# Performance work log

Hardware: AMD Instinct MI355X
Metric: run time of the kernel (lower is better)

Reference implementation:

```python
import jax, jax.numpy as jnp
import numpy as np

K_NEIGHBORS = 32
BN_EPS = 1e-5


def setup_inputs() -> dict:
    key = jax.random.key(0)
    ks = jax.random.split(key, 5)
    B, N, C, OUT = 16, 2048, 3, 32
    x = jax.random.normal(ks[0], (B, N, C), dtype=jnp.float32)
    W1 = jax.random.normal(ks[1], (2 * C, 2 * C), dtype=jnp.float32) * 0.3
    b1 = jax.random.normal(ks[2], (2 * C,), dtype=jnp.float32) * 0.05
    W2 = jax.random.normal(ks[3], (2 * C, OUT), dtype=jnp.float32) * 0.3
    b2 = jax.random.normal(ks[4], (OUT,), dtype=jnp.float32) * 0.05
    return {
        "x": x,
        "W1": W1, "b1": b1,
        "gamma1": jnp.ones((2 * C,), jnp.float32), "beta1": jnp.zeros((2 * C,), jnp.float32),
        "W2": W2, "b2": b2,
        "gamma2": jnp.ones((OUT,), jnp.float32), "beta2": jnp.zeros((OUT,), jnp.float32),
    }


def _batchnorm_train(h, gamma, beta):
    # normalize over all axes except the last (channel) axis, biased variance
    axes = tuple(range(h.ndim - 1))
    mean = jnp.mean(h, axis=axes)
    var = jnp.var(h, axis=axes)
    return gamma * (h - mean) * jax.lax.rsqrt(var + BN_EPS) + beta


def reference(x, W1, b1, gamma1, beta1, W2, b2, gamma2, beta2):
    B, N, C = x.shape
    K = min(K_NEIGHBORS, N)
    # brute-force KNN: squared euclidean distances [B,N,N]
    sq = jnp.sum(x * x, axis=-1)
    d = sq[:, :, None] + sq[:, None, :] - 2.0 * jnp.einsum('bnc,bmc->bnm', x, x)
    _, idx = jax.lax.top_k(-d, K)  # [B,N,K] nearest (self first)
    # gather neighbor points: [B,N,K,C]
    knn = jax.vmap(lambda pts, i: pts[i])(x, idx)
    diffs = x[:, :, None, :] - knn
    h = jnp.concatenate([jnp.broadcast_to(x[:, :, None, :], (B, N, K, C)), diffs], axis=-1)  # [B,N,K,2C]
    h = jax.nn.elu(_batchnorm_train(h @ W1 + b1, gamma1, beta1))
    h = jnp.max(h, axis=2)  # max-pool over K neighbors -> [B,N,2C]
    y = jax.nn.elu(_batchnorm_train(h @ W2 + b2, gamma2, beta2))
    return y
```

## Files before the change

### kernel.cpp

```cpp
#include <hip/hip_runtime.h>
#include <math.h>

namespace {
constexpr int NB = 16, NP = 2048, KNN = 32, CH1 = 6, CH2 = 32;
constexpr int QPB = 8;
constexpr int NBLK = NB * NP / QPB;
constexpr float BN_EPS = 1e-5f;

constexpr size_t OFF_S1REP   = 0;
constexpr size_t OFF_STATS2L = 768;
constexpr size_t OFF_SC1     = 1664;
constexpr size_t OFF_P       = 2048;
constexpr size_t OFF_MINQ    = OFF_P + sizeof(float)*NB*NP*CH1;
}

typedef __attribute__((ext_vector_type(2))) float f32x2;

__device__ __forceinline__ f32x2 pk_mul(f32x2 a, f32x2 b) {
  f32x2 d; asm("v_pk_mul_f32 %0, %1, %2" : "=v"(d) : "v"(a), "v"(b)); return d;
}
__device__ __forceinline__ f32x2 pk_add(f32x2 a, f32x2 b) {
  f32x2 d; asm("v_pk_add_f32 %0, %1, %2" : "=v"(d) : "v"(a), "v"(b)); return d;
}

template <int C> __device__ __forceinline__ int dpp0i(int x) {
  return __builtin_amdgcn_update_dpp(0, x, C, 0xf, 0xf, true);
}
template <int C> __device__ __forceinline__ float dpp0f(float x) {
  return __uint_as_float((unsigned)__builtin_amdgcn_update_dpp(
      0, (int)__float_as_uint(x), C, 0xf, 0xf, true));
}
template <int C> __device__ __forceinline__ float dppInff(float x) {
  return __uint_as_float((unsigned)__builtin_amdgcn_update_dpp(
      0x7F800000, (int)__float_as_uint(x), C, 0xf, 0xf, false));
}
__device__ __forceinline__ int wave_isum_bcast(int x) {
  x += dpp0i<0x111>(x); x += dpp0i<0x112>(x); x += dpp0i<0x114>(x);
  x += dpp0i<0x118>(x); x += dpp0i<0x142>(x); x += dpp0i<0x143>(x);
  return __builtin_amdgcn_readlane(x, 63);
}
__device__ __forceinline__ float wave_fsum63(float x) {
  x += dpp0f<0x111>(x); x += dpp0f<0x112>(x); x += dpp0f<0x114>(x);
  x += dpp0f<0x118>(x); x += dpp0f<0x142>(x); x += dpp0f<0x143>(x);
  return x;
}
__device__ __forceinline__ float wave_fmin63(float x) {
  x = fminf(x, dppInff<0x111>(x)); x = fminf(x, dppInff<0x112>(x));
  x = fminf(x, dppInff<0x114>(x)); x = fminf(x, dppInff<0x118>(x));
  x = fminf(x, dppInff<0x142>(x)); x = fminf(x, dppInff<0x143>(x));
  return x;
}

#define BSEL(m, x, y) ((((x)) & (m)) | (((y)) & ~(m)))

#define RROUND(alive, below, rem, ca, plane)                  \
  { unsigned z_ = BSEL((plane), 0u, (alive));                 \
    int c_ = wave_isum_bcast(__popc(z_));                     \
    if (c_ >= (rem)) { alive = z_; ca = c_; }                 \
    else { rem -= c_; below |= z_; alive &= (plane); ca -= c_; } }

#define RPAIR(alive, below, rem, ca, p0, p1)                                   \
  { unsigned a0_  = BSEL((p0), 0u, (alive));                                   \
    unsigned a1_  = (alive) & (p0);                                            \
    unsigned z00_ = BSEL((p1), 0u, a0_);                                       \
    unsigned z01_ = a0_ & (p1);                                                \
    unsigned z10_ = BSEL((p1), 0u, a1_);                                       \
    unsigned z11_ = a1_ & (p1);                                                \
    int c00_ = wave_isum_bcast(__popc(z00_));                                  \
    int c01_ = wave_isum_bcast(__popc(z01_));                                  \
    int c10_ = wave_isum_bcast(__popc(z10_));                                  \
    if (c00_ >= (rem)) { alive = z00_; ca = c00_; }                            \
    else if (c00_ + c01_ >= (rem)) {                                           \
      below |= z00_; rem -= c00_; alive = z01_; ca = c01_;                     \
    } else if (c00_ + c01_ + c10_ >= (rem)) {                                  \
      below |= z00_ | z01_; rem -= c00_ + c01_; alive = z10_; ca = c10_;       \
    } else {                                                                   \
      below |= z00_ | z01_ | z10_; rem -= c00_ + c01_ + c10_;                  \
      alive = z11_; ca = (ca) - c00_ - c01_ - c10_;                            \
    } }

#define TR16(a)                                                      \
  _Pragma("unroll") for (int g_ = 0; g_ < 8; ++g_) {                 \
    unsigned hi_ = a[g_], lo_ = a[g_+8];                             \
    a[g_]   = __builtin_amdgcn_perm(hi_, lo_, 0x07030501u);          \
    a[g_+8] = __builtin_amdgcn_perm(hi_, lo_, 0x06020400u); }        \
  _Pragma("unroll") for (int g_ = 0; g_ < 8; ++g_) {                 \
    int k_ = (g_ >> 2)*8 + (g_ & 3);                                 \
    unsigned A_ = a[k_], B_ = a[k_+4];                               \
    a[k_]   = BSEL(0x0F0F0F0Fu, B_ >> 4, A_);                        \
    a[k_+4] = BSEL(0xF0F0F0F0u, A_ << 4, B_); }                      \
  _Pragma("unroll") for (int g_ = 0; g_ < 8; ++g_) {                 \
    int k_ = (g_ >> 1)*4 + (g_ & 1);                                 \
    unsigned A_ = a[k_], B_ = a[k_+2];                               \
    a[k_]   = BSEL(0x33333333u, B_ >> 2, A_);                        \
    a[k_+2] = BSEL(0xCCCCCCCCu, A_ << 2, B_); }                      \
  _Pragma("unroll") for (int g_ = 0; g_ < 8; ++g_) {                 \
    int k_ = g_*2;                                                   \
    unsigned A_ = a[k_], B_ = a[k_+1];                               \
    a[k_]   = BSEL(0x55555555u, B_ >> 1, A_);                        \
    a[k_+1] = BSEL(0xAAAAAAAAu, A_ << 1, B_); }

__global__ __launch_bounds__(512, 8) void knn_kernel(const float* __restrict__ x,
                                                     const float* __restrict__ W1,
                                                     const float* __restrict__ b1,
                                                     float* __restrict__ pout,
                                                     float* __restrict__ minq,
                                                     double* __restrict__ s1rep) {
  __shared__ float4 XC[512], YC[512], ZC[512], WC[512];
  __shared__ float red[12][QPB];
  const int lane = threadIdx.x & 63;
  const int w    = threadIdx.x >> 6;
  const int qi   = blockIdx.x * QPB + w;
  const int b    = qi >> 11;
  const int n    = qi & (NP - 1);

  const float* xb = x + (size_t)b * NP * 3;
  {
    const int t = threadIdx.x;
    const int g0 = t >> 6, ls = t & 63;
    float xx[4], yy[4], zz[4], ww[4];
#pragma unroll
    for (int k = 0; k < 4; ++k) {
      const float* pp = xb + (g0*256 + k*64 + ls) * 3;
      float a0 = pp[0], a1 = pp[1], a2 = pp[2];
      xx[k] = a0; yy[k] = a1; zz[k] = a2;
      ww[k] = __fadd_rn(__fadd_rn(__fmul_rn(a0,a0), __fmul_rn(a1,a1)), __fmul_rn(a2,a2));
    }
    XC[t] = (float4){xx[0], xx[1], xx[2], xx[3]};
    YC[t] = (float4){yy[0], yy[1], yy[2], yy[3]};
    ZC[t] = (float4){zz[0], zz[1], zz[2], zz[3]};
    WC[t] = (float4){ww[0], ww[1], ww[2], ww[3]};
  }
  __syncthreads();

  const float* Xs = (const float*)XC;
  const float* Ys = (const float*)YC;
  const float* Zs = (const float*)ZC;
  const float* Ws = (const float*)WC;

  const int vq = n >> 6, lq = n & 63;
  const int qidx = (((vq >> 2) << 6) | lq) * 4 + (vq & 3);
  const float qx = Xs[qidx], qy = Ys[qidx], qz = Zs[qidx], qw = Ws[qidx];
  const f32x2 qx2 = {qx,qx}, qy2 = {qy,qy}, qz2 = {qz,qz}, qw2 = {qw,qw};

  unsigned dd[32];
#pragma unroll
  for (int g = 0; g < 8; ++g) {
    const int cs = g*64 + lane;
    float4 X = XC[cs], Y = YC[cs], Z = ZC[cs], Wv = WC[cs];
    f32x2 x01 = {X.x,X.y}, y01 = {Y.x,Y.y}, z01 = {Z.x,Z.y}, w01 = {Wv.x,Wv.y};
    f32x2 x23 = {X.z,X.w}, y23 = {Y.z,Y.w}, z23 = {Z.z,Z.w}, w23 = {Wv.z,Wv.w};
    f32x2 dotA = pk_add(pk_add(pk_mul(qx2,x01), pk_mul(qy2,y01)), pk_mul(qz2,z01));
    f32x2 dotB = pk_add(pk_add(pk_mul(qx2,x23), pk_mul(qy2,y23)), pk_mul(qz2,z23));
    f32x2 ssA = pk_add(qw2, w01), ssB = pk_add(qw2, w23);
    f32x2 dA = pk_add(dotA, dotA), dB = pk_add(dotB, dotB);
    dd[31-(4*g+0)] = __float_as_uint(__fsub_rn(ssA.x, dA.x));
    dd[31-(4*g+1)] = __float_as_uint(__fsub_rn(ssA.y, dA.y));
    dd[31-(4*g+2)] = __float_as_uint(__fsub_rn(ssB.x, dB.x));
    dd[31-(4*g+3)] = __float_as_uint(__fsub_rn(ssB.y, dB.y));
  }

  unsigned h[16], l[16];
#pragma unroll
  for (int g = 0; g < 16; ++g) {
    h[g] = __builtin_amdgcn_perm(dd[g], dd[g+16], 0x07060302u);
    l[g] = __builtin_amdgcn_perm(dd[g], dd[g+16], 0x05040100u);
  }
  TR16(h);

  unsigned alive = 0xFFFFFFFFu, below = 0u;
  int rem = KNN, ca = 2048;
  RPAIR(alive, below, rem, ca, h[1],  h[2]);
  RPAIR(alive, below, rem, ca, h[3],  h[4]);
  RPAIR(alive, below, rem, ca, h[5],  h[6]);
  if (ca != rem) RPAIR(alive, below, rem, ca, h[7],  h[8]);
  if (ca != rem) RPAIR(alive, below, rem, ca, h[9],  h[10]);
  if (ca != rem) RPAIR(alive, below, rem, ca, h[11], h[12]);
  if (ca != rem) RPAIR(alive, below, rem, ca, h[13], h[14]);
  if (ca != rem) RROUND(alive, below, rem, ca, h[15]);

  unsigned sel;
  if (__builtin_expect(ca == rem, 1)) {
    sel = below | alive;
  } else {
    TR16(l);
#pragma unroll
    for (int i = 0; i < 16; ++i) {
      if (ca != rem) RROUND(alive, below, rem, ca, l[i]);
    }
    sel = below;
    if (ca == rem) {
      sel |= alive;
    } else {
      for (int v = 0; v < 32; ++v) {
        if (rem <= 0) break;
        bool mine = (alive >> v) & 1;
        unsigned long long mb = __ballot(mine);
        int c = __popcll(mb);
        if (c <= rem) { if (mine) sel |= 1u << v; rem -= c; }
        else {
          if (mine && (int)__popcll(mb & ((1ull << lane) - 1)) < rem) sel |= 1u << v;
          rem = 0;
        }
      }
    }
  }

  float w3[CH1], w4[CH1], w5[CH1];
#pragma unroll
  for (int c = 0; c < CH1; ++c) { w3[c]=W1[3*CH1+c]; w4[c]=W1[4*CH1+c]; w5[c]=W1[5*CH1+c]; }
  float sq_[CH1], sqq[CH1], mn[CH1];
#pragma unroll
  for (int c = 0; c < CH1; ++c) { sq_[c] = 0.f; sqq[c] = 0.f; mn[c] = INFINITY; }
  unsigned m = sel;
  while (m) {
    int v = __builtin_ctz(m); m &= m - 1;
    int idx = (((v >> 2) << 6) | lane) * 4 + (v & 3);
    float px_ = Xs[idx], py_ = Ys[idx], pz_ = Zs[idx];
#pragma unroll
    for (int c = 0; c < CH1; ++c) {
      float qv = px_*w3[c] + py_*w4[c] + pz_*w5[c];
      sq_[c] += qv; sqq[c] += qv*qv; mn[c] = fminf(mn[c], qv);
    }
  }

  float pv[CH1];
#pragma unroll
  for (int c = 0; c < CH1; ++c) {
    float qv = qx*w3[c] + qy*w4[c] + qz*w5[c];
    pv[c] = b1[c] + qx*W1[c] + qy*W1[CH1+c] + qz*W1[2*CH1+c] + qv;
  }

#pragma unroll
  for (int c = 0; c < CH1; ++c) {
    float s  = wave_fsum63(sq_[c]);
    float s2 = wave_fsum63(sqq[c]);
    float mm = wave_fmin63(mn[c]);
    if (lane == 63) {
      minq[qi*CH1 + c] = mm;
      red[c][w]       = fmaf(32.f, pv[c], -s);
      red[CH1 + c][w] = fmaf(32.f, pv[c]*pv[c], fmaf(-2.f*pv[c], s, s2));
    }
  }
  if (lane == 0) {
#pragma unroll
    for (int c = 0; c < CH1; ++c) pout[qi*CH1 + c] = pv[c];
  }
  __syncthreads();
  if (threadIdx.x < 12) {
    float s = 0.f;
#pragma unroll
    for (int ww2 = 0; ww2 < QPB; ++ww2) s += red[threadIdx.x][ww2];
    atomicAdd(s1rep + (blockIdx.x & 7) * 12 + threadIdx.x, (double)s);
  }
}

__global__ __launch_bounds__(256) void stage2_kernel(const float* __restrict__ p,
                                                     const float* __restrict__ minq,
                                                     const double* __restrict__ s1rep,
                                                     const float* __restrict__ gamma1,
                                                     const float* __restrict__ beta1,
                                                     float* __restrict__ sc1g,
                                                     double* __restrict__ stats2L) {
  __shared__ double tot1[12];
  __shared__ float sc1s[12];
  __shared__ float acc[4][27];
  const int t = threadIdx.x;
  if (t < 12) {
    double s = 0.0;
#pragma unroll
    for (int r = 0; r < 8; ++r) s += s1rep[r*12 + t];
    tot1[t] = s;
  }
  __syncthreads();
  if (t < CH1) {
    double cnt  = (double)NB * NP * KNN;
    double mean = tot1[t] / cnt;
    double var  = tot1[CH1 + t] / cnt - mean * mean;
    float scale = gamma1[t] / sqrtf((float)var + BN_EPS);
    sc1s[t] = scale; sc1s[CH1 + t] = beta1[t] - (float)mean * scale;
  }
  __syncthreads();
  if (blockIdx.x == 0 && t < 12) sc1g[t] = sc1s[t];

  const int qi = blockIdx.x * 256 + t;
  const int w = t >> 6, lane = t & 63;
  float me[CH1];
#pragma unroll
  for (int c = 0; c < CH1; ++c) {
    float v = fmaf(sc1s[c], p[qi*CH1 + c] - minq[qi*CH1 + c], sc1s[CH1 + c]);
    me[c] = v > 0.f ? v : expm1f(v);
  }
  float vals[27];
#pragma unroll
  for (int c = 0; c < CH1; ++c) vals[c] = me[c];
  {
    int id = 6;
#pragma unroll
    for (int c = 0; c < CH1; ++c)
#pragma unroll
      for (int d = c; d < CH1; ++d) { vals[id] = me[c]*me[d]; ++id; }
  }
#pragma unroll
  for (int k = 0; k < 27; ++k) {
    float s = wave_fsum63(vals[k]);
    if (lane == 63) acc[w][k] = s;
  }
  __syncthreads();
  if (t < 27)
    atomicAdd(stats2L + (blockIdx.x & 3) * 27 + t,
              (double)((acc[0][t] + acc[1][t]) + (acc[2][t] + acc[3][t])));
}

__global__ __launch_bounds__(256) void out_kernel(const float* __restrict__ p,
                                                  const float* __restrict__ minq,
                                                  const float* __restrict__ sc1,
                                                  const float* __restrict__ W2,
                                                  const float* __restrict__ b2,
                                                  const double* __restrict__ stats2L,
                                                  const float* __restrict__ gamma2,
                                                  const float* __restrict__ beta2,
                                                  float* __restrict__ out) {
  __shared__ float m2[27];
  __shared__ float me_lds[8][CH1];
  __shared__ float s2s[CH2], s2h[CH2];
  const int t = threadIdx.x;
  if (t < 27)
    m2[t] = (float)(((stats2L[t] + stats2L[27+t]) + (stats2L[54+t] + stats2L[81+t])));
  const int qbase = blockIdx.x * 8;
  if (t >= 64 && t < 112) {
    int qs = (t - 64) / 6, c = (t - 64) % 6;
    int qi = qbase + qs;
    float v = fmaf(sc1[c], p[qi*CH1 + c] - minq[qi*CH1 + c], sc1[CH1 + c]);
    me_lds[qs][c] = v > 0.f ? v : expm1f(v);
  }
  __syncthreads();
  if (t < CH2) {
    float wv[CH1];
#pragma unroll
    for (int c = 0; c < CH1; ++c) wv[c] = W2[c*CH2 + t];
    float sy = 0.f;
#pragma unroll
    for (int c = 0; c < CH1; ++c) sy = fmaf(wv[c], m2[c], sy);
    float sy2 = 0.f;
    {
      int id = 6;
#pragma unroll
      for (int c = 0; c < CH1; ++c)
#pragma unroll
        for (int d = c; d < CH1; ++d) {
          float coef = (c == d) ? wv[c]*wv[c] : 2.f*wv[c]*wv[d];
          sy2 = fmaf(coef, m2[id], sy2); ++id;
        }
    }
    const double N = (double)NB * NP;
    double bo   = (double)b2[t];
    double mean = ((double)sy + N*bo) / N;
    double Ey2  = ((double)sy2 + 2.0*bo*(double)sy + N*bo*bo) / N;
    double var  = Ey2 - mean*mean;
    float scale = gamma2[t] / sqrtf((float)var + BN_EPS);
    s2s[t] = scale; s2h[t] = beta2[t] - (float)mean * scale;
  }
  __syncthreads();
  const int qs = t >> 5, o = t & 31;
  const int qi = qbase + qs;
  float y = b2[o];
#pragma unroll
  for (int c = 0; c < CH1; ++c) y = fmaf(me_lds[qs][c], W2[c*CH2 + o], y);
  float r = fmaf(s2s[o], y, s2h[o]);
  out[(size_t)qi*CH2 + o] = r > 0.f ? r : expm1f(r);
}

extern "C" void kernel_launch(void* const* d_in, const int* in_sizes, int n_in,
                              void* d_out, int out_size, void* d_ws, size_t ws_size,
                              hipStream_t stream) {
  const float* x      = (const float*)d_in[0];
  const float* W1     = (const float*)d_in[1];
  const float* b1     = (const float*)d_in[2];
  const float* gamma1 = (const float*)d_in[3];
  const float* beta1  = (const float*)d_in[4];
  const float* W2     = (const float*)d_in[5];
  const float* b2     = (const float*)d_in[6];
  const float* gamma2 = (const float*)d_in[7];
  const float* beta2  = (const float*)d_in[8];
  float* out = (float*)d_out;
  char* ws = (char*)d_ws;

  double* s1rep   = (double*)(ws + OFF_S1REP);
  double* stats2L = (double*)(ws + OFF_STATS2L);
  float* sc1  = (float*)(ws + OFF_SC1);
  float* p    = (float*)(ws + OFF_P);
  float* minq = (float*)(ws + OFF_MINQ);

  hipMemsetAsync(ws, 0, 1664, stream);

  knn_kernel   <<<dim3(NBLK),       dim3(512), 0, stream>>>(x, W1, b1, p, minq, s1rep);
  stage2_kernel<<<dim3(NB*NP/256),  dim3(256), 0, stream>>>(p, minq, s1rep, gamma1, beta1,
                                                            sc1, stats2L);
  out_kernel   <<<dim3(NB*NP/8),    dim3(256), 0, stream>>>(p, minq, sc1, W2, b2,
                                                            stats2L, gamma2, beta2, out);
}
```

Baseline: 83.52 us.

## Process two query phases per KNN block and replace pair-radix rounds with single rounds

Each block now handles 16 queries in two sequential phases of 8 waves. The shared-memory point tile is loaded once and reused for both phases, and the number of blocks and atomics is halved. The paired radix-select rounds (RPAIR) are replaced by single-bit RROUND steps, and the occupancy hint drops from 8 to 6. The goal is to amortize the tile load and the atomic reduction, at the cost of fewer blocks for latency hiding and more reduction rounds in the select.

Result: slower. 91.93 us (+10.1%).

```diff
diff --git a/kernel.cpp b/kernel.cpp
--- a/kernel.cpp
+++ b/kernel.cpp
@@ -3,7 +3,7 @@
 
 namespace {
 constexpr int NB = 16, NP = 2048, KNN = 32, CH1 = 6, CH2 = 32;
-constexpr int QPB = 8;
+constexpr int QPB = 16;
 constexpr int NBLK = NB * NP / QPB;
 constexpr float BN_EPS = 1e-5f;
 
@@ -58,26 +58,6 @@
     int c_ = wave_isum_bcast(__popc(z_));                     \
     if (c_ >= (rem)) { alive = z_; ca = c_; }                 \
     else { rem -= c_; below |= z_; alive &= (plane); ca -= c_; } }
-
-#define RPAIR(alive, below, rem, ca, p0, p1)                                   \
-  { unsigned a0_  = BSEL((p0), 0u, (alive));                                   \
-    unsigned a1_  = (alive) & (p0);                                            \
-    unsigned z00_ = BSEL((p1), 0u, a0_);                                       \
-    unsigned z01_ = a0_ & (p1);                                                \
-    unsigned z10_ = BSEL((p1), 0u, a1_);                                       \
-    unsigned z11_ = a1_ & (p1);                                                \
-    int c00_ = wave_isum_bcast(__popc(z00_));                                  \
-    int c01_ = wave_isum_bcast(__popc(z01_));                                  \
-    int c10_ = wave_isum_bcast(__popc(z10_));                                  \
-    if (c00_ >= (rem)) { alive = z00_; ca = c00_; }                            \
-    else if (c00_ + c01_ >= (rem)) {                                           \
-      below |= z00_; rem -= c00_; alive = z01_; ca = c01_;                     \
-    } else if (c00_ + c01_ + c10_ >= (rem)) {                                  \
-      below |= z00_ | z01_; rem -= c00_ + c01_; alive = z10_; ca = c10_;       \
-    } else {                                                                   \
-      below |= z00_ | z01_ | z10_; rem -= c00_ + c01_ + c10_;                  \
-      alive = z11_; ca = (ca) - c00_ - c01_ - c10_;                            \
-    } }
 
 #define TR16(a)                                                      \
   _Pragma("unroll") for (int g_ = 0; g_ < 8; ++g_) {                 \
@@ -100,19 +80,18 @@
     a[k_]   = BSEL(0x55555555u, B_ >> 1, A_);                        \
     a[k_+1] = BSEL(0xAAAAAAAAu, A_ << 1, B_); }
 
-__global__ __launch_bounds__(512, 8) void knn_kernel(const float* __restrict__ x,
+__global__ __launch_bounds__(512, 6) void knn_kernel(const float* __restrict__ x,
                                                      const float* __restrict__ W1,
                                                      const float* __restrict__ b1,
                                                      float* __restrict__ pout,
                                                      float* __restrict__ minq,
                                                      double* __restrict__ s1rep) {
   __shared__ float4 XC[512], YC[512], ZC[512], WC[512];
-  __shared__ float red[12][QPB];
-  const int lane = threadIdx.x & 63;
-  const int w    = threadIdx.x >> 6;
-  const int qi   = blockIdx.x * QPB + w;
-  const int b    = qi >> 11;
-  const int n    = qi & (NP - 1);
+  __shared__ float red[12][8];
+  const int lane  = threadIdx.x & 63;
+  const int w     = threadIdx.x >> 6;
+  const int qbase = blockIdx.x * QPB;
+  const int b     = qbase >> 11;
 
   const float* xb = x + (size_t)b * NP * 3;
   {
@@ -138,119 +117,133 @@
   const float* Zs = (const float*)ZC;
   const float* Ws = (const float*)WC;
 
-  const int vq = n >> 6, lq = n & 63;
-  const int qidx = (((vq >> 2) << 6) | lq) * 4 + (vq & 3);
-  const float qx = Xs[qidx], qy = Ys[qidx], qz = Zs[qidx], qw = Ws[qidx];
-  const f32x2 qx2 = {qx,qx}, qy2 = {qy,qy}, qz2 = {qz,qz}, qw2 = {qw,qw};
-
-  unsigned dd[32];
-#pragma unroll
-  for (int g = 0; g < 8; ++g) {
-    const int cs = g*64 + lane;
-    float4 X = XC[cs], Y = YC[cs], Z = ZC[cs], Wv = WC[cs];
-    f32x2 x01 = {X.x,X.y}, y01 = {Y.x,Y.y}, z01 = {Z.x,Z.y}, w01 = {Wv.x,Wv.y};
-    f32x2 x23 = {X.z,X.w}, y23 = {Y.z,Y.w}, z23 = {Z.z,Z.w}, w23 = {Wv.z,Wv.w};
-    f32x2 dotA = pk_add(pk_add(pk_mul(qx2,x01), pk_mul(qy2,y01)), pk_mul(qz2,z01));
-    f32x2 dotB = pk_add(pk_add(pk_mul(qx2,x23), pk_mul(qy2,y23)), pk_mul(qz2,z23));
-    f32x2 ssA = pk_add(qw2, w01), ssB = pk_add(qw2, w23);
-    f32x2 dA = pk_add(dotA, dotA), dB = pk_add(dotB, dotB);
-    dd[31-(4*g+0)] = __float_as_uint(__fsub_rn(ssA.x, dA.x));
-    dd[31-(4*g+1)] = __float_as_uint(__fsub_rn(ssA.y, dA.y));
-    dd[31-(4*g+2)] = __float_as_uint(__fsub_rn(ssB.x, dB.x));
-    dd[31-(4*g+3)] = __float_as_uint(__fsub_rn(ssB.y, dB.y));
-  }
-
-  unsigned h[16], l[16];
-#pragma unroll
-  for (int g = 0; g < 16; ++g) {
-    h[g] = __builtin_amdgcn_perm(dd[g], dd[g+16], 0x07060302u);
-    l[g] = __builtin_amdgcn_perm(dd[g], dd[g+16], 0x05040100u);
-  }
-  TR16(h);
-
-  unsigned alive = 0xFFFFFFFFu, below = 0u;
-  int rem = KNN, ca = 2048;
-  RPAIR(alive, below, rem, ca, h[1],  h[2]);
-  RPAIR(alive, below, rem, ca, h[3],  h[4]);
-  RPAIR(alive, below, rem, ca, h[5],  h[6]);
-  if (ca != rem) RPAIR(alive, below, rem, ca, h[7],  h[8]);
-  if (ca != rem) RPAIR(alive, below, rem, ca, h[9],  h[10]);
-  if (ca != rem) RPAIR(alive, below, rem, ca, h[11], h[12]);
-  if (ca != rem) RPAIR(alive, below, rem, ca, h[13], h[14]);
-  if (ca != rem) RROUND(alive, below, rem, ca, h[15]);
-
-  unsigned sel;
-  if (__builtin_expect(ca == rem, 1)) {
-    sel = below | alive;
-  } else {
-    TR16(l);
-#pragma unroll
-    for (int i = 0; i < 16; ++i) {
-      if (ca != rem) RROUND(alive, below, rem, ca, l[i]);
-    }
-    sel = below;
-    if (ca == rem) {
-      sel |= alive;
+  float hsAcc[CH1], hqAcc[CH1];
+#pragma unroll
+  for (int c = 0; c < CH1; ++c) { hsAcc[c] = 0.f; hqAcc[c] = 0.f; }
+
+#pragma unroll 1
+  for (int ph = 0; ph < 2; ++ph) {
+    const int qi = qbase + ph * 8 + w;
+    const int n  = qi & (NP - 1);
+
+    const int vq = n >> 6, lq = n & 63;
+    const int qidx = (((vq >> 2) << 6) | lq) * 4 + (vq & 3);
+    const float qx = Xs[qidx], qy = Ys[qidx], qz = Zs[qidx], qw = Ws[qidx];
+    const f32x2 qx2 = {qx,qx}, qy2 = {qy,qy}, qz2 = {qz,qz}, qw2 = {qw,qw};
+
+    unsigned dd[32];
+#pragma unroll
+    for (int g = 0; g < 8; ++g) {
+      const int cs = g*64 + lane;
+      float4 X = XC[cs], Y = YC[cs], Z = ZC[cs], Wv = WC[cs];
+      f32x2 x01 = {X.x,X.y}, y01 = {Y.x,Y.y}, z01 = {Z.x,Z.y}, w01 = {Wv.x,Wv.y};
+      f32x2 x23 = {X.z,X.w}, y23 = {Y.z,Y.w}, z23 = {Z.z,Z.w}, w23 = {Wv.z,Wv.w};
+      f32x2 dotA = pk_add(pk_add(pk_mul(qx2,x01), pk_mul(qy2,y01)), pk_mul(qz2,z01));
+      f32x2 dotB = pk_add(pk_add(pk_mul(qx2,x23), pk_mul(qy2,y23)), pk_mul(qz2,z23));
+      f32x2 ssA = pk_add(qw2, w01), ssB = pk_add(qw2, w23);
+      f32x2 dA = pk_add(dotA, dotA), dB = pk_add(dotB, dotB);
+      dd[31-(4*g+0)] = __float_as_uint(__fsub_rn(ssA.x, dA.x));
+      dd[31-(4*g+1)] = __float_as_uint(__fsub_rn(ssA.y, dA.y));
+      dd[31-(4*g+2)] = __float_as_uint(__fsub_rn(ssB.x, dB.x));
+      dd[31-(4*g+3)] = __float_as_uint(__fsub_rn(ssB.y, dB.y));
+    }
+
+    unsigned h[16], l[16];
+#pragma unroll
+    for (int g = 0; g < 16; ++g) {
+      h[g] = __builtin_amdgcn_perm(dd[g], dd[g+16], 0x07060302u);
+      l[g] = __builtin_amdgcn_perm(dd[g], dd[g+16], 0x05040100u);
+    }
+    TR16(h);
+
+    unsigned alive = 0xFFFFFFFFu, below = 0u;
+    int rem = KNN, ca = 2048;
+#pragma unroll
+    for (int i = 1; i <= 6; ++i) {
+      RROUND(alive, below, rem, ca, h[i]);
+    }
+#pragma unroll
+    for (int i = 7; i <= 15; ++i) {
+      if (ca != rem) RROUND(alive, below, rem, ca, h[i]);
+    }
+    unsigned sel;
+    if (__builtin_expect(ca == rem, 1)) {
+      sel = below | alive;
     } else {
-      for (int v = 0; v < 32; ++v) {
-        if (rem <= 0) break;
-        bool mine = (alive >> v) & 1;
-        unsigned long long mb = __ballot(mine);
-        int c = __popcll(mb);
-        if (c <= rem) { if (mine) sel |= 1u << v; rem -= c; }
-        else {
-          if (mine && (int)__popcll(mb & ((1ull << lane) - 1)) < rem) sel |= 1u << v;
-          rem = 0;
+      TR16(l);
+#pragma unroll
+      for (int i = 0; i < 16; ++i) {
+        if (ca != rem) RROUND(alive, below, rem, ca, l[i]);
+      }
+      sel = below;
+      if (ca == rem) {
+        sel |= alive;
+      } else {
+        for (int v = 0; v < 32; ++v) {
+          if (rem <= 0) break;
+          bool mine = (alive >> v) & 1;
+          unsigned long long mb = __ballot(mine);
+          int c = __popcll(mb);
+          if (c <= rem) { if (mine) sel |= 1u << v; rem -= c; }
+          else {
+            if (mine && (int)__popcll(mb & ((1ull << lane) - 1)) < rem) sel |= 1u << v;
+            rem = 0;
+          }
         }
       }
     }
-  }
-
-  float w3[CH1], w4[CH1], w5[CH1];
-#pragma unroll
-  for (int c = 0; c < CH1; ++c) { w3[c]=W1[3*CH1+c]; w4[c]=W1[4*CH1+c]; w5[c]=W1[5*CH1+c]; }
-  float sq_[CH1], sqq[CH1], mn[CH1];
-#pragma unroll
-  for (int c = 0; c < CH1; ++c) { sq_[c] = 0.f; sqq[c] = 0.f; mn[c] = INFINITY; }
-  unsigned m = sel;
-  while (m) {
-    int v = __builtin_ctz(m); m &= m - 1;
-    int idx = (((v >> 2) << 6) | lane) * 4 + (v & 3);
-    float px_ = Xs[idx], py_ = Ys[idx], pz_ = Zs[idx];
+
+    float w3[CH1], w4[CH1], w5[CH1];
+#pragma unroll
+    for (int c = 0; c < CH1; ++c) { w3[c]=W1[3*CH1+c]; w4[c]=W1[4*CH1+c]; w5[c]=W1[5*CH1+c]; }
+    float sq_[CH1], sqq[CH1], mn[CH1];
+#pragma unroll
+    for (int c = 0; c < CH1; ++c) { sq_[c] = 0.f; sqq[c] = 0.f; mn[c] = INFINITY; }
+    unsigned m = sel;
+    while (m) {
+      int v = __builtin_ctz(m); m &= m - 1;
+      int idx = (((v >> 2) << 6) | lane) * 4 + (v & 3);
+      float px_ = Xs[idx], py_ = Ys[idx], pz_ = Zs[idx];
+#pragma unroll
+      for (int c = 0; c < CH1; ++c) {
+        float qv = px_*w3[c] + py_*w4[c] + pz_*w5[c];
+        sq_[c] += qv; sqq[c] += qv*qv; mn[c] = fminf(mn[c], qv);
+      }
+    }
+
+    float pv[CH1];
 #pragma unroll
     for (int c = 0; c < CH1; ++c) {
-      float qv = px_*w3[c] + py_*w4[c] + pz_*w5[c];
-      sq_[c] += qv; sqq[c] += qv*qv; mn[c] = fminf(mn[c], qv);
-    }
-  }
-
-  float pv[CH1];
-#pragma unroll
-  for (int c = 0; c < CH1; ++c) {
-    float qv = qx*w3[c] + qy*w4[c] + qz*w5[c];
-    pv[c] = b1[c] + qx*W1[c] + qy*W1[CH1+c] + qz*W1[2*CH1+c] + qv;
-  }
-
-#pragma unroll
-  for (int c = 0; c < CH1; ++c) {
-    float s  = wave_fsum63(sq_[c]);
-    float s2 = wave_fsum63(sqq[c]);
-    float mm = wave_fmin63(mn[c]);
-    if (lane == 63) {
-      minq[qi*CH1 + c] = mm;
-      red[c][w]       = fmaf(32.f, pv[c], -s);
-      red[CH1 + c][w] = fmaf(32.f, pv[c]*pv[c], fmaf(-2.f*pv[c], s, s2));
-    }
-  }
-  if (lane == 0) {
-#pragma unroll
-    for (int c = 0; c < CH1; ++c) pout[qi*CH1 + c] = pv[c];
+      float qv = qx*w3[c] + qy*w4[c] + qz*w5[c];
+      pv[c] = b1[c] + qx*W1[c] + qy*W1[CH1+c] + qz*W1[2*CH1+c] + qv;
+    }
+
+#pragma unroll
+    for (int c = 0; c < CH1; ++c) {
+      float s  = wave_fsum63(sq_[c]);
+      float s2 = wave_fsum63(sqq[c]);
+      float mm = wave_fmin63(mn[c]);
+      if (lane == 63) {
+        minq[qi*CH1 + c] = mm;
+        hsAcc[c] += fmaf(32.f, pv[c], -s);
+        hqAcc[c] += fmaf(32.f, pv[c]*pv[c], fmaf(-2.f*pv[c], s, s2));
+      }
+    }
+    if (lane == 0) {
+#pragma unroll
+      for (int c = 0; c < CH1; ++c) pout[qi*CH1 + c] = pv[c];
+    }
+  }
+
+  if (lane == 63) {
+#pragma unroll
+    for (int c = 0; c < CH1; ++c) { red[c][w] = hsAcc[c]; red[CH1 + c][w] = hqAcc[c]; }
   }
   __syncthreads();
   if (threadIdx.x < 12) {
     float s = 0.f;
 #pragma unroll
-    for (int ww2 = 0; ww2 < QPB; ++ww2) s += red[threadIdx.x][ww2];
+    for (int ww2 = 0; ww2 < 8; ++ww2) s += red[threadIdx.x][ww2];
     atomicAdd(s1rep + (blockIdx.x & 7) * 12 + threadIdx.x, (double)s);
   }
 }
```
